# Optimization experiments

Hardware: AMD Instinct MI355X
Metric: run time of the kernel (lower is better)

## Reference

```python
import jax, jax.numpy as jnp
import numpy as np

HEADS = 8
DIM_HEAD = 64

def setup_inputs() -> dict:
    key = jax.random.key(0)
    ks = jax.random.split(key, 9)
    B, N1, N2, D = 4, 2048, 2048, 1024
    inner = HEADS * DIM_HEAD  # 512
    s_in = 1.0 / np.sqrt(D)
    s_inner = 1.0 / np.sqrt(inner)
    return {
        "x1": jax.random.normal(ks[0], (B, N1, D), jnp.float32),
        "x2": jax.random.normal(ks[1], (B, N2, D), jnp.float32),
        "Wq1": jax.random.normal(ks[2], (D, inner), jnp.float32) * s_in,
        "Wk1": jax.random.normal(ks[3], (D, inner), jnp.float32) * s_in,
        "Wv1": jax.random.normal(ks[4], (D, inner), jnp.float32) * s_in,
        "Wk2": jax.random.normal(ks[5], (D, inner), jnp.float32) * s_in,
        "Wv2": jax.random.normal(ks[6], (D, inner), jnp.float32) * s_in,
        "Wo": jax.random.normal(ks[7], (inner, D), jnp.float32) * s_inner,
        "bo": jnp.zeros((D,), jnp.float32),
    }

def reference(x1, x2, Wq1, Wk1, Wv1, Wk2, Wv2, Wo, bo):
    h, d = HEADS, DIM_HEAD
    scale = d ** (-0.5)
    B, N1, _ = x1.shape
    N2 = x2.shape[1]

    def split_heads(t, n):
        return t.reshape(B, n, h, d)  # [B, n, h, d]

    q1 = split_heads(x1 @ Wq1, N1)
    k1 = split_heads(x1 @ Wk1, N1)
    v1 = split_heads(x1 @ Wv1, N1)
    k2 = split_heads(x2 @ Wk2, N2)
    v2 = split_heads(x2 @ Wv2, N2)

    k = jnp.concatenate([k1, k2], axis=1)  # [B, N1+N2, h, d]
    v = jnp.concatenate([v1, v2], axis=1)

    # fp32 precision for QK^T (matches _ATTN_PRECISION == 'fp32')
    sim = jnp.einsum('bihd,bjhd->bhij', q1.astype(jnp.float32),
                     k.astype(jnp.float32)) * scale  # [B, h, N1, N1+N2]
    attn = jax.nn.softmax(sim, axis=-1)
    out = jnp.einsum('bhij,bjhd->bihd', attn, v)  # [B, N1, h, d]
    out = out.reshape(B, N1, h * d)
    return out @ Wo + bo
```

## Files before the change

### kernel.cpp

```cpp
#include <hip/hip_runtime.h>
#include <stdint.h>

typedef __bf16 bf16x8 __attribute__((ext_vector_type(8)));
typedef float f32x4 __attribute__((ext_vector_type(4)));
typedef unsigned short ushort_t;

#define MFMA16(a,b,c) __builtin_amdgcn_mfma_f32_16x16x32_bf16((a),(b),(c),0,0,0)

__device__ __forceinline__ unsigned short f2bf(float f){
    unsigned u = __builtin_bit_cast(unsigned, f);
    u += 0x7fffu + ((u>>16)&1u);
    return (unsigned short)(u>>16);
}
__device__ __forceinline__ unsigned pack2bf(float lo, float hi){
    unsigned a = __builtin_bit_cast(unsigned, lo) + 0x8000u;
    unsigned b = __builtin_bit_cast(unsigned, hi) + 0x8000u;
    return __builtin_amdgcn_perm(b, a, 0x07060302u);
}
__device__ __forceinline__ float bflo(unsigned u){
    return __builtin_bit_cast(float, u << 16);
}
__device__ __forceinline__ float bfhi(unsigned u){
    return __builtin_bit_cast(float, u & 0xffff0000u);
}
__device__ __forceinline__ float fexp2(float x){
#if __has_builtin(__builtin_amdgcn_exp2f)
    return __builtin_amdgcn_exp2f(x);
#else
    return exp2f(x);
#endif
}

__device__ __forceinline__ void async16(ushort_t* lds, const ushort_t* g){
#if __has_builtin(__builtin_amdgcn_global_load_lds)
    __builtin_amdgcn_global_load_lds(
        (const __attribute__((address_space(1))) void*)g,
        (__attribute__((address_space(3))) void*)lds, 16, 0, 0);
#else
    const int l = (int)(threadIdx.x & 63u);
    *(uint4*)(lds + (size_t)l*8) = *(const uint4*)g;
#endif
}

__global__ __launch_bounds__(256) void prep_all(
    const float* __restrict__ x1, const float* __restrict__ x2,
    const float* __restrict__ w0, const float* __restrict__ w1,
    const float* __restrict__ w2, const float* __restrict__ w3,
    const float* __restrict__ w4, const float* __restrict__ wo,
    ushort_t* __restrict__ Xc1, ushort_t* __restrict__ Xc2,
    ushort_t* __restrict__ Wt1, ushort_t* __restrict__ Wt2,
    ushort_t* __restrict__ Wot)
{
    __shared__ float Tb[64*33];
    const int bid = blockIdx.x;
    const int t = threadIdx.x;
    if (bid < 8192) {
        const float* src = (bid >= 4096) ? x2 : x1;
        ushort_t*    dst = (bid >= 4096) ? Xc2 : Xc1;
        size_t i = ((size_t)(bid & 4095)*256 + t)*8;
        float4 a = *(const float4*)(src + i);
        float4 b = *(const float4*)(src + i + 4);
        uint4 o;
        o.x = pack2bf(a.x, a.y); o.y = pack2bf(a.z, a.w);
        o.z = pack2bf(b.x, b.y); o.w = pack2bf(b.z, b.w);
        *(uint4*)(dst + i) = o;
    } else if (bid < 10752) {
        const int r = bid - 8192;
        const int z = r >> 9;
        const int rr = r & 511;
        const int k0 = (rr & 31)*32, n0 = (rr >> 5)*32;
        const float* src; ushort_t* dst;
        if (z < 3)  { src = (z==0)?w0:((z==1)?w1:w2); dst = Wt1 + (size_t)z*512*1024; }
        else        { src = (z==3)?w3:w4;             dst = Wt2 + (size_t)(z-3)*512*1024; }
        const int N = 512, K = 1024;
        int kr = t>>3, nc = (t&7)*4;
        float4 v = *(const float4*)(src + (size_t)(k0+kr)*N + n0 + nc);
        Tb[kr*33+nc] = v.x; Tb[kr*33+nc+1] = v.y;
        Tb[kr*33+nc+2] = v.z; Tb[kr*33+nc+3] = v.w;
        __syncthreads();
        int nr = t>>3, kc = (t&7)*4;
        uint2 o;
        o.x = pack2bf(Tb[kc*33+nr],     Tb[(kc+1)*33+nr]);
        o.y = pack2bf(Tb[(kc+2)*33+nr], Tb[(kc+3)*33+nr]);
        *(uint2*)(dst + (size_t)(n0+nr)*K + k0 + kc) = o;
    } else {
        const int r = bid - 10752;
        const int k0 = (r & 7)*64;
        const int n0 = (r >> 3)*32;
        const int kr = t>>3, nc = (t&7)*4;
#pragma unroll
        for (int hf = 0; hf < 2; ++hf){
            float4 v = *(const float4*)(wo + (size_t)(k0 + hf*32 + kr)*1024 + n0 + nc);
            Tb[(hf*32+kr)*33+nc]   = v.x; Tb[(hf*32+kr)*33+nc+1] = v.y;
            Tb[(hf*32+kr)*33+nc+2] = v.z; Tb[(hf*32+kr)*33+nc+3] = v.w;
        }
        __syncthreads();
        const int nr = t>>3, kc = (t&7)*8;
        ushort_t tmp[8];
#pragma unroll
        for (int e = 0; e < 8; ++e){
            int dp = kc + e;
            int d  = ((dp&3)<<4) | (dp>>2);
            tmp[e] = f2bf(Tb[d*33+nr]);
        }
        *(uint4*)(Wot + (size_t)(n0+nr)*512 + k0 + kc) = *(uint4*)tmp;
    }
}

__global__ __launch_bounds__(256, 4) void qkv_gemm(
    const ushort_t* __restrict__ A1, const ushort_t* __restrict__ A2,
    const ushort_t* __restrict__ B1, const ushort_t* __restrict__ B2,
    ushort_t* __restrict__ Qp, ushort_t* __restrict__ Kp, ushort_t* __restrict__ Vtp)
{
    constexpr int KD = 1024;
    __shared__ ushort_t As[2][128][32];
    __shared__ ushort_t Bs[2][128][32];
    const int yb = blockIdx.y;
    const bool second = (yb >= 12);
    const ushort_t* A  = second ? A2 : A1;
    const ushort_t* Bt = second ? B2 : B1;
    const int n0 = (second ? (yb-12) : yb) * 128;
    const int koff = second ? 2048 : 0;
    const int sub  = second ? (1 + (n0>>9)) : (n0>>9);

    const int t = threadIdx.x;
    const int m0 = blockIdx.x*128;
    const int w = t>>6, l = t&63;
    const int quad = l>>4, lc = l&15;
    const int wr = (w>>1)*64, wc = (w&1)*64;

    f32x4 acc[4][4] = {};

    const int crow = l>>2;
    const int kseg = (l&3)*8;
    const ushort_t* gA0 = A  + (size_t)(m0 + w*32      + crow)*KD + kseg;
    const ushort_t* gA1 = A  + (size_t)(m0 + w*32 + 16 + crow)*KD + kseg;
    const ushort_t* gB0 = Bt + (size_t)(n0 + w*32      + crow)*KD + kseg;
    const ushort_t* gB1 = Bt + (size_t)(n0 + w*32 + 16 + crow)*KD + kseg;

    const int NK = KD/32;

    async16(&As[0][w*32][0],    gA0);
    async16(&As[0][w*32+16][0], gA1);
    async16(&Bs[0][w*32][0],    gB0);
    async16(&Bs[0][w*32+16][0], gB1);
    __syncthreads();

    for (int kk = 0; kk < NK; ++kk) {
        const int cur = kk & 1;
        if (kk + 1 < NK) {
            const int k0 = (kk+1)*32;
            const int nx = cur ^ 1;
            async16(&As[nx][w*32][0],    gA0 + k0);
            async16(&As[nx][w*32+16][0], gA1 + k0);
            async16(&Bs[nx][w*32][0],    gB0 + k0);
            async16(&Bs[nx][w*32+16][0], gB1 + k0);
        }
        bf16x8 af[4], bfv[4];
#pragma unroll
        for (int i = 0; i < 4; ++i) {
            af[i]  = *(const bf16x8*)&As[cur][wr + i*16 + lc][quad*8];
            bfv[i] = *(const bf16x8*)&Bs[cur][wc + i*16 + lc][quad*8];
        }
#pragma unroll
        for (int mt = 0; mt < 4; ++mt)
#pragma unroll
            for (int nt = 0; nt < 4; ++nt)
                acc[mt][nt] = MFMA16(af[mt], bfv[nt], acc[mt][nt]);
        __syncthreads();
    }

    const int hh  = ((n0 + wc)>>6) & 7;
    const int dp  = 4*lc;
    const float QSC = 0.18033688011112042f;
    if (sub == 0) {
#pragma unroll
        for (int mt = 0; mt < 4; ++mt) {
            const int row = m0 + wr + mt*16 + quad*4;
            const int b = row>>11, i = row & 2047;
#pragma unroll
            for (int r = 0; r < 4; ++r) {
                uint2 o;
                o.x = pack2bf(acc[mt][0][r]*QSC, acc[mt][1][r]*QSC);
                o.y = pack2bf(acc[mt][2][r]*QSC, acc[mt][3][r]*QSC);
                *(uint2*)(Qp + ((size_t)(b*8+hh)*2048 + i + r)*64 + dp) = o;
            }
        }
    } else if (sub == 1) {
#pragma unroll
        for (int mt = 0; mt < 4; ++mt) {
            const int row = m0 + wr + mt*16 + quad*4;
            const int b = row>>11, i = row & 2047;
#pragma unroll
            for (int r = 0; r < 4; ++r) {
                uint2 o;
                o.x = pack2bf(acc[mt][0][r], acc[mt][1][r]);
                o.y = pack2bf(acc[mt][2][r], acc[mt][3][r]);
                *(uint2*)(Kp + ((size_t)(b*8+hh)*4096 + koff + i + r)*64 + dp) = o;
            }
        }
    } else {
#pragma unroll
        for (int mt = 0; mt < 4; ++mt) {
            const int row = m0 + wr + mt*16 + quad*4;
            const int b = row>>11, i = row & 2047;
            const int ip = (i & ~28) | (((i>>2)&3)<<3) | (((i>>4)&1)<<2);
#pragma unroll
            for (int nt = 0; nt < 4; ++nt) {
                uint2 o;
                o.x = pack2bf(acc[mt][nt][0], acc[mt][nt][1]);
                o.y = pack2bf(acc[mt][nt][2], acc[mt][nt][3]);
                *(uint2*)(Vtp + ((size_t)(b*8+hh)*64 + dp + nt)*4096 + koff + ip) = o;
            }
        }
    }
}

__global__ __launch_bounds__(256, 4) void out_gemm(
    const ushort_t* __restrict__ A, const ushort_t* __restrict__ Bt,
    float* __restrict__ outF, const float* __restrict__ bias)
{
    constexpr int KD = 512;
    __shared__ ushort_t As[2][128][32];
    __shared__ ushort_t Bs[2][128][32];
    const int t = threadIdx.x;
    const int m0 = blockIdx.x*128, n0 = blockIdx.y*128;
    const int w = t>>6, l = t&63;
    const int quad = l>>4, lc = l&15;
    const int wr = (w>>1)*64, wc = (w&1)*64;

    f32x4 acc[4][4] = {};

    const int crow = l>>2;
    const int kseg = (l&3)*8;
    const ushort_t* gA0 = A  + (size_t)(m0 + w*32      + crow)*KD + kseg;
    const ushort_t* gA1 = A  + (size_t)(m0 + w*32 + 16 + crow)*KD + kseg;
    const ushort_t* gB0 = Bt + (size_t)(n0 + w*32      + crow)*KD + kseg;
    const ushort_t* gB1 = Bt + (size_t)(n0 + w*32 + 16 + crow)*KD + kseg;

    const int NK = KD/32;

    async16(&As[0][w*32][0],    gA0);
    async16(&As[0][w*32+16][0], gA1);
    async16(&Bs[0][w*32][0],    gB0);
    async16(&Bs[0][w*32+16][0], gB1);
    __syncthreads();

    for (int kk = 0; kk < NK; ++kk) {
        const int cur = kk & 1;
        if (kk + 1 < NK) {
            const int k0 = (kk+1)*32;
            const int nx = cur ^ 1;
            async16(&As[nx][w*32][0],    gA0 + k0);
            async16(&As[nx][w*32+16][0], gA1 + k0);
            async16(&Bs[nx][w*32][0],    gB0 + k0);
            async16(&Bs[nx][w*32+16][0], gB1 + k0);
        }
        bf16x8 af[4], bfv[4];
#pragma unroll
        for (int i = 0; i < 4; ++i) {
            af[i]  = *(const bf16x8*)&As[cur][wr + i*16 + lc][quad*8];
            bfv[i] = *(const bf16x8*)&Bs[cur][wc + i*16 + lc][quad*8];
        }
#pragma unroll
        for (int mt = 0; mt < 4; ++mt)
#pragma unroll
            for (int nt = 0; nt < 4; ++nt)
                acc[mt][nt] = MFMA16(af[mt], bfv[nt], acc[mt][nt]);
        __syncthreads();
    }

    float bv[4];
#pragma unroll
    for (int nt = 0; nt < 4; ++nt) bv[nt] = bias[n0 + wc + nt*16 + lc];
#pragma unroll
    for (int mt = 0; mt < 4; ++mt) {
        const int row = m0 + wr + mt*16 + quad*4;
#pragma unroll
        for (int nt = 0; nt < 4; ++nt) {
            const int col = n0 + wc + nt*16 + lc;
#pragma unroll
            for (int r = 0; r < 4; ++r)
                outF[(size_t)(row+r)*1024 + col] = acc[mt][nt][r] + bv[nt];
        }
    }
}

template<int SPLIT>
__global__ __launch_bounds__(256, 4) void flash_attn_k(
    const ushort_t* __restrict__ Q, const ushort_t* __restrict__ Kg,
    const ushort_t* __restrict__ Vt, ushort_t* __restrict__ AO,
    ushort_t* __restrict__ P0, ushort_t* __restrict__ P1, float* __restrict__ Lp)
{
    constexpr int NJT = 64 / SPLIT;
    __shared__ ushort_t Ks[2][64][64];
    __shared__ ushort_t Vs[2][64][64];
    const int bh = blockIdx.x, qt = blockIdx.y;
    const int sp = (SPLIT > 1) ? (int)blockIdx.z : 0;
    const int jt0 = sp * NJT;
    const int b = bh>>3, h = bh&7;
    const int t = threadIdx.x, wv = t>>6, l = t&63;
    const int quad = l>>4, lc = l&15;

    const ushort_t* qbase = Q + ((size_t)bh*2048 + qt*128 + wv*16 + lc)*64;
    bf16x8 qA0 = *(const bf16x8*)(qbase + quad*8);
    bf16x8 qA1 = *(const bf16x8*)(qbase + 32 + quad*8);
    bf16x8 qB0 = *(const bf16x8*)(qbase + 64*64 + quad*8);
    bf16x8 qB1 = *(const bf16x8*)(qbase + 64*64 + 32 + quad*8);

    const ushort_t* Kb = Kg + (size_t)bh*4096*64;
    const ushort_t* Vb = Vt + (size_t)bh*64*4096;

    const int r8 = l>>3;
    const int sc = (l&7) ^ r8;
    const ushort_t* kg0 = Kb + ((size_t)jt0*64 + wv*16 + r8)*64 + sc*8;
    const ushort_t* kg1 = kg0 + (size_t)8*64;
    const ushort_t* vg0 = Vb + (size_t)(wv*16 + r8)*4096 + (size_t)jt0*64 + sc*8;
    const ushort_t* vg1 = vg0 + (size_t)8*4096;

    const int swA = ((quad       ^ (lc&7)) << 3);
    const int swB = (((quad ^ 4) ^ (lc&7)) << 3);

    float l0 = 0.0f, l1 = 0.0f;
    f32x4 o0[4] = {}, o1[4] = {};

    async16(&Ks[0][wv*16][0],   kg0);
    async16(&Ks[0][wv*16+8][0], kg1);
    async16(&Vs[0][wv*16][0],   vg0);
    async16(&Vs[0][wv*16+8][0], vg1);
    __syncthreads();

    for (int jt = 0; jt < NJT; ++jt) {
        const int cur = jt & 1;
        if (jt + 1 < NJT) {
            const int nx = cur ^ 1;
            const size_t ko = (size_t)(jt+1)*4096;
            const size_t vo = (size_t)(jt+1)*64;
            async16(&Ks[nx][wv*16][0],   kg0 + ko);
            async16(&Ks[nx][wv*16+8][0], kg1 + ko);
            async16(&Vs[nx][wv*16][0],   vg0 + vo);
            async16(&Vs[nx][wv*16+8][0], vg1 + vo);
        }
        const ushort_t* KsC = &Ks[cur][0][0];
        const ushort_t* VsC = &Vs[cur][0][0];

        union { unsigned u[8]; bf16x8 v[2]; } p0, p1;
        float rs0 = 0.0f, rs1 = 0.0f;
#pragma unroll
        for (int kt = 0; kt < 4; ++kt) {
            const int ro = (kt*16 + lc)*64;
            bf16x8 kf0 = *(const bf16x8*)(KsC + ro + swA);
            bf16x8 kf1 = *(const bf16x8*)(KsC + ro + swB);
            f32x4 z0 = {}, z1 = {};
            __builtin_amdgcn_s_setprio(1);
            z0 = MFMA16(kf0, qA0, z0); z0 = MFMA16(kf1, qA1, z0);
            z1 = MFMA16(kf0, qB0, z1); z1 = MFMA16(kf1, qB1, z1);
            __builtin_amdgcn_s_setprio(0);
            float a0 = fexp2(z0[0]), a1v = fexp2(z0[1]);
            float a2 = fexp2(z0[2]), a3 = fexp2(z0[3]);
            rs0 += (a0 + a1v) + (a2 + a3);
            p0.u[kt*2]   = pack2bf(a0, a1v);
            p0.u[kt*2+1] = pack2bf(a2, a3);
            float c0 = fexp2(z1[0]), c1 = fexp2(z1[1]);
            float c2 = fexp2(z1[2]), c3 = fexp2(z1[3]);
            rs1 += (c0 + c1) + (c2 + c3);
            p1.u[kt*2]   = pack2bf(c0, c1);
            p1.u[kt*2+1] = pack2bf(c2, c3);
        }
        l0 += rs0; l1 += rs1;

#pragma unroll
        for (int dt = 0; dt < 4; ++dt) {
            const int ro = (dt*16 + lc)*64;
            bf16x8 vf0 = *(const bf16x8*)(VsC + ro + swA);
            bf16x8 vf1 = *(const bf16x8*)(VsC + ro + swB);
            __builtin_amdgcn_s_setprio(1);
            o0[dt] = MFMA16(vf0, p0.v[0], o0[dt]);
            o0[dt] = MFMA16(vf1, p0.v[1], o0[dt]);
            o1[dt] = MFMA16(vf0, p1.v[0], o1[dt]);
            o1[dt] = MFMA16(vf1, p1.v[1], o1[dt]);
            __builtin_amdgcn_s_setprio(0);
        }
        __syncthreads();
    }

    l0 += __shfl_xor(l0, 16); l0 += __shfl_xor(l0, 32);
    l1 += __shfl_xor(l1, 16); l1 += __shfl_xor(l1, 32);
    float li0 = 1.0f / l0, li1 = 1.0f / l1;

    if (SPLIT == 1) {
        const int qA = qt*128 + wv*16 + lc;
        ushort_t* aodA = AO + ((size_t)b*2048 + qA)*512 + h*64 + quad*4;
        ushort_t* aodB = aodA + (size_t)64*512;
#pragma unroll
        for (int dt = 0; dt < 4; ++dt) {
            uint2 oa, ob;
            oa.x = pack2bf(o0[dt][0]*li0, o0[dt][1]*li0);
            oa.y = pack2bf(o0[dt][2]*li0, o0[dt][3]*li0);
            *(uint2*)(aodA + dt*16) = oa;
            ob.x = pack2bf(o1[dt][0]*li1, o1[dt][1]*li1);
            ob.y = pack2bf(o1[dt][2]*li1, o1[dt][3]*li1);
            *(uint2*)(aodB + dt*16) = ob;
        }
    } else {
        ushort_t* P = sp ? P1 : P0;
        const int bid = bh*16 + qt;
        const int qrA = wv*16 + lc;
        const size_t pbA = ((size_t)bid*128 + qrA)*64;
        const size_t pbB = pbA + (size_t)64*64;
#pragma unroll
        for (int dt = 0; dt < 4; ++dt) {
            uint2 oa, ob;
            oa.x = pack2bf(o0[dt][0]*li0, o0[dt][1]*li0);
            oa.y = pack2bf(o0[dt][2]*li0, o0[dt][3]*li0);
            *(uint2*)(P + pbA + dt*16 + quad*4) = oa;
            ob.x = pack2bf(o1[dt][0]*li1, o1[dt][1]*li1);
            ob.y = pack2bf(o1[dt][2]*li1, o1[dt][3]*li1);
            *(uint2*)(P + pbB + dt*16 + quad*4) = ob;
        }
        if (l < 16) {
            Lp[((size_t)sp*512 + bid)*128 + qrA]      = l0;
            Lp[((size_t)sp*512 + bid)*128 + 64 + qrA] = l1;
        }
    }
}

__global__ __launch_bounds__(256) void combine_attn(
    const ushort_t* __restrict__ P0, const ushort_t* __restrict__ P1,
    const float* __restrict__ Lp, ushort_t* __restrict__ AO)
{
    const int bid = blockIdx.x;
    const int bh = bid>>4, qt = bid&15;
    const int b = bh>>3, h = bh&7;
    const int t = threadIdx.x;
    const int dcol = (t&15)*4;
    const size_t pblk = (size_t)bid*8192;
#pragma unroll
    for (int e = 0; e < 8; ++e) {
        const int qrow = e*16 + (t>>4);
        const size_t idx = pblk + (size_t)qrow*64 + dcol;
        uint2 ua = *(const uint2*)(P0 + idx);
        uint2 ub = *(const uint2*)(P1 + idx);
        float l0 = Lp[(size_t)bid*128 + qrow];
        float l1 = Lp[(size_t)(512 + bid)*128 + qrow];
        float inv = 1.0f / (l0 + l1);
        float w0 = l0*inv, w1 = l1*inv;
        float r0 = w0*bflo(ua.x) + w1*bflo(ub.x);
        float r1 = w0*bfhi(ua.x) + w1*bfhi(ub.x);
        float r2 = w0*bflo(ua.y) + w1*bflo(ub.y);
        float r3 = w0*bfhi(ua.y) + w1*bfhi(ub.y);
        uint2 o;
        o.x = pack2bf(r0, r1);
        o.y = pack2bf(r2, r3);
        ushort_t* ao = AO + ((size_t)b*2048 + qt*128 + qrow)*512 + h*64 + dcol;
        *(uint2*)ao = o;
    }
}

extern "C" void kernel_launch(void* const* d_in, const int* in_sizes, int n_in,
                              void* d_out, int out_size, void* d_ws, size_t ws_size,
                              hipStream_t stream)
{
    const float* x1  = (const float*)d_in[0];
    const float* x2  = (const float*)d_in[1];
    const float* Wq1 = (const float*)d_in[2];
    const float* Wk1 = (const float*)d_in[3];
    const float* Wv1 = (const float*)d_in[4];
    const float* Wk2 = (const float*)d_in[5];
    const float* Wv2 = (const float*)d_in[6];
    const float* Wo  = (const float*)d_in[7];
    const float* bo  = (const float*)d_in[8];
    float* out = (float*)d_out;

    ushort_t* ws  = (ushort_t*)d_ws;
    ushort_t* Xc1 = ws;
    ushort_t* Xc2 = Xc1 + 8388608;
    ushort_t* Wt1 = Xc2 + 8388608;
    ushort_t* Wt2 = Wt1 + 1572864;
    ushort_t* Wot = Wt2 + 1048576;
    ushort_t* Qp  = Wot + 524288;
    ushort_t* Kp  = Qp  + 4194304;
    ushort_t* Vtp = Kp  + 8388608;
    ushort_t* Pex = Vtp + 8388608;
    ushort_t* Lex = Pex + 8388608;
    ushort_t* AOp = Xc2;

    prep_all<<<11008, 256, 0, stream>>>(x1, x2, Wq1, Wk1, Wv1, Wk2, Wv2, Wo,
                                        Xc1, Xc2, Wt1, Wt2, Wot);

    qkv_gemm<<<dim3(64,20), 256, 0, stream>>>(Xc1, Xc2, Wt1, Wt2, Qp, Kp, Vtp);

    const size_t NEED = 99090432ull;
    if (ws_size >= NEED) {
        ushort_t* P0b = Xc1;
        ushort_t* P1b = Pex;
        float*    Lf  = (float*)Lex;
        flash_attn_k<2><<<dim3(32,16,2), 256, 0, stream>>>(Qp, Kp, Vtp, nullptr, P0b, P1b, Lf);
        combine_attn<<<512, 256, 0, stream>>>(P0b, P1b, Lf, AOp);
    } else {
        flash_attn_k<1><<<dim3(32,16,1), 256, 0, stream>>>(Qp, Kp, Vtp, AOp, nullptr, nullptr, nullptr);
    }

    out_gemm<<<dim3(64,8), 256, 0, stream>>>(AOp, Wot, out, bo);
}
```

Baseline: 288.5 us.

## Split attention KV into four chunks with smaller KV tiles and swizzled grid

The flash attention kernel now works on 32-key tiles instead of 64, which halves the shared-memory footprint, and raises the launch bound to 8 blocks per CU. The KV sequence is split four ways instead of two, and a flat grid with a swizzled block index groups blocks sharing a head for L2 locality. The combine kernel now merges four partial outputs, and the softmax sums are stored in the weight-transpose workspace region, which shrinks the workspace requirement. The cost is more partial-output traffic, a heavier combine step, and less work per tile to hide synchronisation.

```diff
diff --git a/kernel.cpp b/kernel.cpp
--- a/kernel.cpp
+++ b/kernel.cpp
@@ -287,16 +287,26 @@
 }
 
 template<int SPLIT>
-__global__ __launch_bounds__(256, 4) void flash_attn_k(
+__global__ __launch_bounds__(256, 8) void flash_attn_k(
     const ushort_t* __restrict__ Q, const ushort_t* __restrict__ Kg,
     const ushort_t* __restrict__ Vt, ushort_t* __restrict__ AO,
-    ushort_t* __restrict__ P0, ushort_t* __restrict__ P1, float* __restrict__ Lp)
+    ushort_t* __restrict__ PA, ushort_t* __restrict__ PB, float* __restrict__ Lp)
 {
-    constexpr int NJT = 64 / SPLIT;
-    __shared__ ushort_t Ks[2][64][64];
-    __shared__ ushort_t Vs[2][64][64];
-    const int bh = blockIdx.x, qt = blockIdx.y;
-    const int sp = (SPLIT > 1) ? (int)blockIdx.z : 0;
+    constexpr int NJT = 128 / SPLIT;
+    __shared__ ushort_t Ks[2][32][64];
+    __shared__ ushort_t Vs[2][64][32];
+
+    int bh, qt, sp;
+    if (SPLIT > 1) {
+        const int id  = (int)blockIdx.x;
+        const int swz = (id & 7)*256 + (id >> 3);
+        bh = swz >> 6;
+        const int rem = swz & 63;
+        sp = rem >> 4;
+        qt = rem & 15;
+    } else {
+        bh = blockIdx.x; qt = blockIdx.y; sp = 0;
+    }
     const int jt0 = sp * NJT;
     const int b = bh>>3, h = bh&7;
     const int t = threadIdx.x, wv = t>>6, l = t&63;
@@ -311,43 +321,38 @@
     const ushort_t* Kb = Kg + (size_t)bh*4096*64;
     const ushort_t* Vb = Vt + (size_t)bh*64*4096;
 
-    const int r8 = l>>3;
-    const int sc = (l&7) ^ r8;
-    const ushort_t* kg0 = Kb + ((size_t)jt0*64 + wv*16 + r8)*64 + sc*8;
-    const ushort_t* kg1 = kg0 + (size_t)8*64;
-    const ushort_t* vg0 = Vb + (size_t)(wv*16 + r8)*4096 + (size_t)jt0*64 + sc*8;
-    const ushort_t* vg1 = vg0 + (size_t)8*4096;
+    const int r8  = l>>3;
+    const int scK = (l&7) ^ r8;
+    const ushort_t* kg = Kb + ((size_t)jt0*32 + wv*8 + r8)*64 + scK*8;
+    const int r16 = l>>2;
+    const int scV = (l&3) ^ ((l>>3)&3);
+    const ushort_t* vg = Vb + (size_t)(wv*16 + r16)*4096 + (size_t)jt0*32 + scV*8;
 
     const int swA = ((quad       ^ (lc&7)) << 3);
     const int swB = (((quad ^ 4) ^ (lc&7)) << 3);
+    const int swV = ((quad ^ ((lc>>1)&3)) << 3);
 
     float l0 = 0.0f, l1 = 0.0f;
     f32x4 o0[4] = {}, o1[4] = {};
 
-    async16(&Ks[0][wv*16][0],   kg0);
-    async16(&Ks[0][wv*16+8][0], kg1);
-    async16(&Vs[0][wv*16][0],   vg0);
-    async16(&Vs[0][wv*16+8][0], vg1);
+    async16(&Ks[0][wv*8][0],  kg);
+    async16(&Vs[0][wv*16][0], vg);
     __syncthreads();
 
     for (int jt = 0; jt < NJT; ++jt) {
         const int cur = jt & 1;
         if (jt + 1 < NJT) {
             const int nx = cur ^ 1;
-            const size_t ko = (size_t)(jt+1)*4096;
-            const size_t vo = (size_t)(jt+1)*64;
-            async16(&Ks[nx][wv*16][0],   kg0 + ko);
-            async16(&Ks[nx][wv*16+8][0], kg1 + ko);
-            async16(&Vs[nx][wv*16][0],   vg0 + vo);
-            async16(&Vs[nx][wv*16+8][0], vg1 + vo);
+            async16(&Ks[nx][wv*8][0],  kg + (size_t)(jt+1)*2048);
+            async16(&Vs[nx][wv*16][0], vg + (size_t)(jt+1)*32);
         }
         const ushort_t* KsC = &Ks[cur][0][0];
         const ushort_t* VsC = &Vs[cur][0][0];
 
-        union { unsigned u[8]; bf16x8 v[2]; } p0, p1;
+        union { unsigned u[4]; bf16x8 v; } p0, p1;
         float rs0 = 0.0f, rs1 = 0.0f;
 #pragma unroll
-        for (int kt = 0; kt < 4; ++kt) {
+        for (int kt = 0; kt < 2; ++kt) {
             const int ro = (kt*16 + lc)*64;
             bf16x8 kf0 = *(const bf16x8*)(KsC + ro + swA);
             bf16x8 kf1 = *(const bf16x8*)(KsC + ro + swB);
@@ -371,14 +376,11 @@
 
 #pragma unroll
         for (int dt = 0; dt < 4; ++dt) {
-            const int ro = (dt*16 + lc)*64;
-            bf16x8 vf0 = *(const bf16x8*)(VsC + ro + swA);
-            bf16x8 vf1 = *(const bf16x8*)(VsC + ro + swB);
+            const int ro = (dt*16 + lc)*32;
+            bf16x8 vf = *(const bf16x8*)(VsC + ro + swV);
             __builtin_amdgcn_s_setprio(1);
-            o0[dt] = MFMA16(vf0, p0.v[0], o0[dt]);
-            o0[dt] = MFMA16(vf1, p0.v[1], o0[dt]);
-            o1[dt] = MFMA16(vf0, p1.v[0], o1[dt]);
-            o1[dt] = MFMA16(vf1, p1.v[1], o1[dt]);
+            o0[dt] = MFMA16(vf, p0.v, o0[dt]);
+            o1[dt] = MFMA16(vf, p1.v, o1[dt]);
             __builtin_amdgcn_s_setprio(0);
         }
         __syncthreads();
@@ -403,7 +405,8 @@
             *(uint2*)(aodB + dt*16) = ob;
         }
     } else {
-        ushort_t* P = sp ? P1 : P0;
+        ushort_t* P = (sp < 2) ? (PA + (size_t)sp*4194304)
+                               : (PB + (size_t)(sp-2)*4194304);
         const int bid = bh*16 + qt;
         const int qrA = wv*16 + lc;
         const size_t pbA = ((size_t)bid*128 + qrA)*64;
@@ -426,7 +429,7 @@
 }
 
 __global__ __launch_bounds__(256) void combine_attn(
-    const ushort_t* __restrict__ P0, const ushort_t* __restrict__ P1,
+    const ushort_t* __restrict__ PA, const ushort_t* __restrict__ PB,
     const float* __restrict__ Lp, ushort_t* __restrict__ AO)
 {
     const int bid = blockIdx.x;
@@ -439,16 +442,20 @@
     for (int e = 0; e < 8; ++e) {
         const int qrow = e*16 + (t>>4);
         const size_t idx = pblk + (size_t)qrow*64 + dcol;
-        uint2 ua = *(const uint2*)(P0 + idx);
-        uint2 ub = *(const uint2*)(P1 + idx);
-        float l0 = Lp[(size_t)bid*128 + qrow];
-        float l1 = Lp[(size_t)(512 + bid)*128 + qrow];
-        float inv = 1.0f / (l0 + l1);
-        float w0 = l0*inv, w1 = l1*inv;
-        float r0 = w0*bflo(ua.x) + w1*bflo(ub.x);
-        float r1 = w0*bfhi(ua.x) + w1*bfhi(ub.x);
-        float r2 = w0*bflo(ua.y) + w1*bflo(ub.y);
-        float r3 = w0*bfhi(ua.y) + w1*bfhi(ub.y);
+        uint2 u0 = *(const uint2*)(PA + idx);
+        uint2 u1 = *(const uint2*)(PA + 4194304 + idx);
+        uint2 u2 = *(const uint2*)(PB + idx);
+        uint2 u3 = *(const uint2*)(PB + 4194304 + idx);
+        float l0 = Lp[(size_t)(0*512 + bid)*128 + qrow];
+        float l1 = Lp[(size_t)(1*512 + bid)*128 + qrow];
+        float l2 = Lp[(size_t)(2*512 + bid)*128 + qrow];
+        float l3 = Lp[(size_t)(3*512 + bid)*128 + qrow];
+        float inv = 1.0f / (l0 + l1 + l2 + l3);
+        float w0 = l0*inv, w1 = l1*inv, w2 = l2*inv, w3 = l3*inv;
+        float r0 = w0*bflo(u0.x) + w1*bflo(u1.x) + w2*bflo(u2.x) + w3*bflo(u3.x);
+        float r1 = w0*bfhi(u0.x) + w1*bfhi(u1.x) + w2*bfhi(u2.x) + w3*bfhi(u3.x);
+        float r2 = w0*bflo(u0.y) + w1*bflo(u1.y) + w2*bflo(u2.y) + w3*bflo(u3.y);
+        float r3 = w0*bfhi(u0.y) + w1*bfhi(u1.y) + w2*bfhi(u2.y) + w3*bfhi(u3.y);
         uint2 o;
         o.x = pack2bf(r0, r1);
         o.y = pack2bf(r2, r3);
@@ -482,7 +489,6 @@
     ushort_t* Kp  = Qp  + 4194304;
     ushort_t* Vtp = Kp  + 8388608;
     ushort_t* Pex = Vtp + 8388608;
-    ushort_t* Lex = Pex + 8388608;
     ushort_t* AOp = Xc2;
 
     prep_all<<<11008, 256, 0, stream>>>(x1, x2, Wq1, Wk1, Wv1, Wk2, Wv2, Wo,
@@ -490,15 +496,15 @@
 
     qkv_gemm<<<dim3(64,20), 256, 0, stream>>>(Xc1, Xc2, Wt1, Wt2, Qp, Kp, Vtp);
 
-    const size_t NEED = 99090432ull;
+    const size_t NEED = 98566144ull;
     if (ws_size >= NEED) {
-        ushort_t* P0b = Xc1;
-        ushort_t* P1b = Pex;
-        float*    Lf  = (float*)Lex;
-        flash_attn_k<2><<<dim3(32,16,2), 256, 0, stream>>>(Qp, Kp, Vtp, nullptr, P0b, P1b, Lf);
-        combine_attn<<<512, 256, 0, stream>>>(P0b, P1b, Lf, AOp);
+        ushort_t* P01 = Xc1;
+        ushort_t* P23 = Pex;
+        float*    Lf  = (float*)Wt1;
+        flash_attn_k<4><<<2048, 256, 0, stream>>>(Qp, Kp, Vtp, nullptr, P01, P23, Lf);
+        combine_attn<<<512, 256, 0, stream>>>(P01, P23, Lf, AOp);
     } else {
-        flash_attn_k<1><<<dim3(32,16,1), 256, 0, stream>>>(Qp, Kp, Vtp, AOp, nullptr, nullptr, nullptr);
+        flash_attn_k<1><<<dim3(32,16), 256, 0, stream>>>(Qp, Kp, Vtp, AOp, nullptr, nullptr, nullptr);
     }
 
     out_gemm<<<dim3(64,8), 256, 0, stream>>>(AOp, Wot, out, bo);
```

New measurement: 721.0 us. 2.5x slower.
